# Kernel tuning notes

Measured on AMD Instinct MI355X. Metric: run time of the kernel, lower is better.

## Reference

```python
import jax, jax.numpy as jnp
import numpy as np

DIM = 2048
KV_DIM = 1024
NUM_HEADS = 16
HEAD_DIM = DIM // NUM_HEADS  # 128
EPS = 1e-6
B, LQ, LKV = 2, 4096, 1024


def _rope_cos_sin(L, d, base=10000.0):
    inv_freq = 1.0 / (base ** (np.arange(0, d, 2, dtype=np.float32) / d))  # [d/2]
    freqs = np.arange(L, dtype=np.float32)[:, None] * inv_freq[None, :]   # [L, d/2]
    emb = np.concatenate([freqs, freqs], axis=-1)                          # [L, d]
    return jnp.asarray(np.cos(emb)), jnp.asarray(np.sin(emb))


def setup_inputs() -> dict:
    key = jax.random.key(0)
    ks = jax.random.split(key, 10)
    x = jax.random.normal(ks[0], (B, LQ, DIM), dtype=jnp.float32)
    y = jax.random.normal(ks[1], (B, LKV, KV_DIM), dtype=jnp.float32)
    xc, xs = _rope_cos_sin(LQ, HEAD_DIM)
    yc, ys = _rope_cos_sin(LKV, HEAD_DIM)
    x_cos = jnp.broadcast_to(xc[None], (B, LQ, HEAD_DIM))
    x_sin = jnp.broadcast_to(xs[None], (B, LQ, HEAD_DIM))
    y_cos = jnp.broadcast_to(yc[None], (B, LKV, HEAD_DIM))
    y_sin = jnp.broadcast_to(ys[None], (B, LKV, HEAD_DIM))
    s = 0.02
    Wq = jax.random.normal(ks[2], (DIM, DIM), dtype=jnp.float32) * s
    Wk = jax.random.normal(ks[3], (DIM, KV_DIM), dtype=jnp.float32) * s
    Wv = jax.random.normal(ks[4], (DIM, KV_DIM), dtype=jnp.float32) * s
    Wo = jax.random.normal(ks[5], (DIM, DIM), dtype=jnp.float32) * s
    bq = jnp.zeros((DIM,), jnp.float32)
    bk = jnp.zeros((DIM,), jnp.float32)
    bv = jnp.zeros((DIM,), jnp.float32)
    bo = jnp.zeros((DIM,), jnp.float32)
    rmsq_w = jnp.ones((DIM,), jnp.float32)
    rmsk_w = jnp.ones((DIM,), jnp.float32)
    ln_w = jnp.ones((KV_DIM,), jnp.float32)
    ln_b = jnp.zeros((KV_DIM,), jnp.float32)
    return dict(x=x, y=y, x_cos=x_cos, x_sin=x_sin, y_cos=y_cos, y_sin=y_sin,
                Wq=Wq, bq=bq, Wk=Wk, bk=bk, Wv=Wv, bv=bv, Wo=Wo, bo=bo,
                rmsq_w=rmsq_w, rmsk_w=rmsk_w, ln_w=ln_w, ln_b=ln_b)


def _rms_norm(t, w, eps=EPS):
    return t * jax.lax.rsqrt(jnp.mean(t * t, axis=-1, keepdims=True) + eps) * w


def _layer_norm(t, w, b, eps=EPS):
    mu = jnp.mean(t, axis=-1, keepdims=True)
    var = jnp.mean(jnp.square(t - mu), axis=-1, keepdims=True)
    return (t - mu) * jax.lax.rsqrt(var + eps) * w + b


def _rotate_half(t):
    d2 = t.shape[-1] // 2
    return jnp.concatenate([-t[..., d2:], t[..., :d2]], axis=-1)


def _apply_rope(t, cos, sin):
    # t: [B, L, H, D]; cos/sin: [B, L, D] -> unsqueeze head dim (unsqueeze_dim=2)
    cos = cos[:, :, None, :]
    sin = sin[:, :, None, :]
    return t * cos + _rotate_half(t) * sin


def _block_forward(x, y, x_cos, x_sin, y_cos, y_sin,
                   Wq, bq, Wk, bk, Wv, bv, Wo, bo,
                   rmsq_w, rmsk_w, ln_w, ln_b):
    Bb, Lq, D = x.shape
    Lk = y.shape[1]
    H, Dh = NUM_HEADS, HEAD_DIM
    # y pre-norm (block-level LayerNorm)
    yn = _layer_norm(y, ln_w, ln_b)
    # projections + RMSNorm on q/k
    q = _rms_norm(x @ Wq.T + bq, rmsq_w)   # [B, Lq, D]
    k = _rms_norm(yn @ Wk.T + bk, rmsk_w)  # [B, Lk, D]
    v = yn @ Wv.T + bv                     # [B, Lk, D]
    # split heads and apply RoPE
    q = _apply_rope(q.reshape(Bb, Lq, H, Dh), x_cos, x_sin)
    k = _apply_rope(k.reshape(Bb, Lk, H, Dh), y_cos, y_sin)
    v = v.reshape(Bb, Lk, H, Dh)
    # non-causal cross attention, scale = 1/sqrt(head_dim)
    scale = 1.0 / jnp.sqrt(jnp.asarray(Dh, q.dtype))
    scores = jnp.einsum('blhd,bmhd->bhlm', q, k) * scale
    probs = jax.nn.softmax(scores, axis=-1)
    out = jnp.einsum('bhlm,bmhd->blhd', probs, v).reshape(Bb, Lq, D)
    return out @ Wo.T + bo


def reference(x, y, x_cos, x_sin, y_cos, y_sin,
              Wq, bq, Wk, bk, Wv, bv, Wo, bo,
              rmsq_w, rmsk_w, ln_w, ln_b):
    return _block_forward(x, y, x_cos, x_sin, y_cos, y_sin,
                          Wq, bq, Wk, bk, Wv, bv, Wo, bo,
                          rmsq_w, rmsk_w, ln_w, ln_b)
```

## Files before the change

### kernel.cpp

```cpp
#include <hip/hip_runtime.h>


typedef __attribute__((ext_vector_type(8))) short    short8;
typedef __attribute__((ext_vector_type(8))) unsigned short ushort8;
typedef __attribute__((ext_vector_type(4))) unsigned short ushort4v;
typedef __attribute__((ext_vector_type(4))) float    f32x4;
typedef __attribute__((ext_vector_type(16))) float   f32x16;
typedef __attribute__((ext_vector_type(4))) unsigned int uint4v;

#define DEV __device__ __forceinline__

DEV unsigned short f2bf(float f) {
  unsigned int u = __builtin_bit_cast(unsigned int, f);
  u += 0x7FFFu + ((u >> 16) & 1u);
  return (unsigned short)(u >> 16);
}
DEV float bf2f(unsigned short h) {
  return __builtin_bit_cast(float, ((unsigned int)h) << 16);
}
DEV unsigned int cvtpk_bf16(float lo, float hi) {
  unsigned int r;
  asm("v_cvt_pk_bf16_f32 %0, %1, %2" : "=v"(r) : "v"(lo), "v"(hi));
  return r;
}
DEV short8 mk8(unsigned a, unsigned b, unsigned c, unsigned d) {
  uint4v t; t.x = a; t.y = b; t.z = c; t.w = d;
  return __builtin_bit_cast(short8, t);
}

DEV void gload_lds16(const void* g, void* l) {
  __builtin_amdgcn_global_load_lds(
      (const __attribute__((address_space(1))) void*)g,
      (__attribute__((address_space(3))) void*)l, 16, 0, 0);
}

__global__ __launch_bounds__(256) void cvt_kernel(const float* __restrict__ in,
                                                  unsigned short* __restrict__ out,
                                                  int n4) {
  int idx = blockIdx.x * 256 + threadIdx.x;
  int stride = gridDim.x * 256;
  for (int i = idx; i < n4; i += stride) {
    float4 v = *(const float4*)(in + (size_t)i * 4);
    ushort4v o;
    o.x = f2bf(v.x); o.y = f2bf(v.y); o.z = f2bf(v.z); o.w = f2bf(v.w);
    *(ushort4v*)(out + (size_t)i * 4) = o;
  }
}

__global__ __launch_bounds__(256) void cvt4_kernel(const float* __restrict__ s0,
                                                   const float* __restrict__ s1,
                                                   const float* __restrict__ s2,
                                                   const float* __restrict__ s3,
                                                   unsigned short* __restrict__ d0,
                                                   unsigned short* __restrict__ d1,
                                                   unsigned short* __restrict__ d2,
                                                   unsigned short* __restrict__ d3,
                                                   int n0, int n1, int n2, int n3) {
  const int total = n0 + n1 + n2 + n3;
  int idx = blockIdx.x * 256 + threadIdx.x;
  const int stride = gridDim.x * 256;
  for (int i = idx; i < total; i += stride) {
    int j = i;
    const float* s; unsigned short* d;
    if (j < n0) { s = s0; d = d0; }
    else if ((j -= n0) < n1) { s = s1; d = d1; }
    else if ((j -= n1) < n2) { s = s2; d = d2; }
    else { j -= n2; s = s3; d = d3; }
    float4 v = *(const float4*)(s + (size_t)j * 4);
    ushort4v o;
    o.x = f2bf(v.x); o.y = f2bf(v.y); o.z = f2bf(v.z); o.w = f2bf(v.w);
    *(ushort4v*)(d + (size_t)j * 4) = o;
  }
}

__global__ __launch_bounds__(256) void ln_kernel(const float* __restrict__ y,
                                                 const float* __restrict__ w,
                                                 const float* __restrict__ b,
                                                 unsigned short* __restrict__ yn) {
  const int row = blockIdx.x;
  const int t = threadIdx.x;
  const float* yr = y + (size_t)row * 1024;
  float4 v = *(const float4*)(yr + t * 4);
  float s1 = v.x + v.y + v.z + v.w;
  float s2 = v.x * v.x + v.y * v.y + v.z * v.z + v.w * v.w;
#pragma unroll
  for (int m = 1; m < 64; m <<= 1) {
    s1 += __shfl_xor(s1, m);
    s2 += __shfl_xor(s2, m);
  }
  __shared__ float red[8];
  const int wave = t >> 6, lane = t & 63;
  if (lane == 0) { red[wave] = s1; red[4 + wave] = s2; }
  __syncthreads();
  s1 = red[0] + red[1] + red[2] + red[3];
  s2 = red[4] + red[5] + red[6] + red[7];
  const float mu = s1 * (1.0f / 1024.0f);
  const float var = s2 * (1.0f / 1024.0f) - mu * mu;
  const float rs = rsqrtf(var + 1e-6f);
  ushort4v o;
  o.x = f2bf((v.x - mu) * rs * w[t * 4 + 0] + b[t * 4 + 0]);
  o.y = f2bf((v.y - mu) * rs * w[t * 4 + 1] + b[t * 4 + 1]);
  o.z = f2bf((v.z - mu) * rs * w[t * 4 + 2] + b[t * 4 + 2]);
  o.w = f2bf((v.w - mu) * rs * w[t * 4 + 3] + b[t * 4 + 3]);
  *(ushort4v*)(yn + (size_t)row * 1024 + t * 4) = o;
}

__global__ __launch_bounds__(256) void gemm_bt(const unsigned short* __restrict__ A,
                                               const unsigned short* __restrict__ W,
                                               const float* __restrict__ bias0,
                                               const float* __restrict__ bias1,
                                               int nsplit,
                                               unsigned short* __restrict__ Cout,
                                               int M, int N, int K) {
  __shared__ __align__(16) char sA[128 * 128];
  __shared__ __align__(16) char sB[128 * 128];
  const int tid = threadIdx.x;
  const int wave = tid >> 6, lane = tid & 63;
  const int lg = lane >> 4, l15 = lane & 15;
  const int wr = wave >> 1, wc = wave & 1;
  const int m0 = blockIdx.y * 128;
  const int n0 = blockIdx.x * 128;
  const char* Ab = (const char*)A;
  const char* Wb = (const char*)W;
  const size_t ldab = (size_t)K * 2;

  f32x4 acc[4][4] = {};

  for (int kt = 0; kt < K; kt += 64) {
#pragma unroll
    for (int i = 0; i < 4; ++i) {
      const int p = (i * 256 + tid) * 16;
      const int row = p >> 7;
      const int si = (p & 127) ^ ((row & 7) << 4);
      gload_lds16(Ab + (size_t)(m0 + row) * ldab + (size_t)kt * 2 + si, sA + p);
    }
#pragma unroll
    for (int i = 0; i < 4; ++i) {
      const int p = (i * 256 + tid) * 16;
      const int row = p >> 7;
      const int si = (p & 127) ^ ((row & 7) << 4);
      gload_lds16(Wb + (size_t)(n0 + row) * ldab + (size_t)kt * 2 + si, sB + p);
    }
    __syncthreads();
#pragma unroll
    for (int ks = 0; ks < 2; ++ks) {
      const int kb = (ks * 32 + lg * 8) * 2;
      short8 af[4], bw[4];
#pragma unroll
      for (int mf = 0; mf < 4; ++mf) {
        const int row = wr * 64 + mf * 16 + l15;
        af[mf] = *(const short8*)(sA + row * 128 + (kb ^ ((row & 7) << 4)));
      }
#pragma unroll
      for (int nf = 0; nf < 4; ++nf) {
        const int row = wc * 64 + nf * 16 + l15;
        bw[nf] = *(const short8*)(sB + row * 128 + (kb ^ ((row & 7) << 4)));
      }
#pragma unroll
      for (int mf = 0; mf < 4; ++mf)
#pragma unroll
        for (int nf = 0; nf < 4; ++nf)
          acc[mf][nf] = __builtin_amdgcn_mfma_f32_16x16x32_bf16(af[mf], bw[nf],
                                                                acc[mf][nf], 0, 0, 0);
    }
    __syncthreads();
  }

#pragma unroll
  for (int nf = 0; nf < 4; ++nf) {
    const int n = n0 + wc * 64 + nf * 16 + l15;
    const float bv = (n < nsplit) ? bias0[n] : bias1[n - nsplit];
#pragma unroll
    for (int mf = 0; mf < 4; ++mf) {
      const int mB = m0 + wr * 64 + mf * 16 + lg * 4;
#pragma unroll
      for (int r = 0; r < 4; ++r)
        Cout[(size_t)(mB + r) * N + n] = f2bf(acc[mf][nf][r] + bv);
    }
  }
}

template <int EPI>
__global__ __launch_bounds__(512, 2) void gemm256(const unsigned short* __restrict__ A,
                                                  const unsigned short* __restrict__ W,
                                                  const float* __restrict__ bias,
                                                  void* __restrict__ Cout,
                                                  int M, int N, int K) {
  __shared__ __align__(16) char lds[2][4][16384];
  const int tid = threadIdx.x;
  const int wave = tid >> 6, lane = tid & 63;
  const int lg = lane >> 4, l15 = lane & 15;
  const int wm = wave >> 2, wn = wave & 3;

  const int nwg = gridDim.x;
  const int wgid = (blockIdx.x & 7) * (nwg >> 3) + (blockIdx.x >> 3);
  const int nbn = N >> 8;
  const int m0 = (wgid / nbn) * 256;
  const int n0 = (wgid % nbn) * 256;

  const char* Ab = (const char*)A;
  const char* Wb = (const char*)W;
  const size_t ld = (size_t)K * 2;
  const int NT = K >> 6;
  const int NI = NT >> 1;

  const int prow = tid >> 3;
  const int psw  = ((tid * 16) & 127) ^ ((prow & 7) << 4);
  const int pdst = tid * 16;
  const char* pAg = Ab + (size_t)(m0 + prow) * ld + psw;
  const char* pBg = Wb + (size_t)(n0 + prow) * ld + psw;

  f32x4 acc[8][4] = {};
  short8 af[4][2];
  short8 bf[4][2];

#define STG(BUF, HALF, ISB, TAU) do {                                         \
    const char* _g = ((ISB) ? pBg : pAg) + (size_t)(HALF) * 128 * ld +        \
                     (size_t)(TAU) * 128;                                     \
    char* _l = lds[BUF][(ISB) * 2 + (HALF)];                                  \
    gload_lds16(_g, _l + pdst);                                               \
    gload_lds16(_g + 64 * ld, _l + pdst + 8192);                              \
  } while (0)

#define LDA(BUF, H) do {                                                      \
    const char* _b = lds[BUF][wm];                                            \
    _Pragma("unroll") for (int mfl = 0; mfl < 4; ++mfl) {                     \
      const int _r = (H) * 64 + mfl * 16 + l15;                               \
      _Pragma("unroll") for (int ks = 0; ks < 2; ++ks)                        \
        af[mfl][ks] = *(const short8*)(_b + _r * 128 +                        \
                        ((ks * 64 + lg * 16) ^ ((_r & 7) << 4)));             \
    }                                                                         \
  } while (0)

#define LDB(BUF, G) do {                                                      \
    const char* _b = lds[BUF][2 + (wn >> 1)];                                 \
    _Pragma("unroll") for (int nfl = 0; nfl < 2; ++nfl) {                     \
      const int _r = (wn & 1) * 64 + (G) * 32 + nfl * 16 + l15;               \
      _Pragma("unroll") for (int ks = 0; ks < 2; ++ks)                        \
        bf[(G) * 2 + nfl][ks] = *(const short8*)(_b + _r * 128 +              \
                        ((ks * 64 + lg * 16) ^ ((_r & 7) << 4)));             \
    }                                                                         \
  } while (0)

#define MFMA_Q(H, G) do {                                                     \
    __builtin_amdgcn_s_setprio(1);                                            \
    _Pragma("unroll") for (int ks = 0; ks < 2; ++ks)                          \
    _Pragma("unroll") for (int mfl = 0; mfl < 4; ++mfl)                       \
    _Pragma("unroll") for (int nfl = 0; nfl < 2; ++nfl)                       \
      acc[(H) * 4 + mfl][(G) * 2 + nfl] =                                     \
        __builtin_amdgcn_mfma_f32_16x16x32_bf16(af[mfl][ks],                  \
            bf[(G) * 2 + nfl][ks], acc[(H) * 4 + mfl][(G) * 2 + nfl], 0,0,0); \
    __builtin_amdgcn_s_setprio(0);                                            \
  } while (0)

#define BAR() __builtin_amdgcn_s_barrier()
#define LGKM0() do { asm volatile("s_waitcnt lgkmcnt(0)" ::: "memory");       \
    __builtin_amdgcn_sched_barrier(0); } while (0)
#define VM4() asm volatile("s_waitcnt vmcnt(4)" ::: "memory")
#define VM0() asm volatile("s_waitcnt vmcnt(0)" ::: "memory")

  STG(0, 0, 0, 0); STG(0, 1, 0, 0); STG(0, 0, 1, 0); STG(0, 1, 1, 0);
  STG(1, 0, 1, 1); STG(1, 1, 1, 1);
  VM4(); BAR();

  for (int t = 0; t < NI - 1; ++t) {
    const int t2 = 2 * t;
    LDA(0, 0); LDB(0, 0); STG(1, 0, 0, t2 + 1);
    BAR(); LGKM0(); MFMA_Q(0, 0); BAR();
    LDB(0, 1); STG(1, 1, 0, t2 + 1);
    BAR(); LGKM0(); MFMA_Q(0, 1); BAR();
    LDA(0, 1); STG(0, 0, 1, t2 + 2);
    BAR(); LGKM0(); MFMA_Q(1, 1); BAR();
    STG(0, 1, 1, t2 + 2);
    BAR(); MFMA_Q(1, 0); VM4(); BAR();
    LDA(1, 0); LDB(1, 0); STG(0, 0, 0, t2 + 2);
    BAR(); LGKM0(); MFMA_Q(0, 0); BAR();
    LDB(1, 1); STG(0, 1, 0, t2 + 2);
    BAR(); LGKM0(); MFMA_Q(0, 1); BAR();
    LDA(1, 1); STG(1, 0, 1, t2 + 3);
    BAR(); LGKM0(); MFMA_Q(1, 1); BAR();
    STG(1, 1, 1, t2 + 3);
    BAR(); MFMA_Q(1, 0); VM4(); BAR();
  }

  LDA(0, 0); LDB(0, 0); STG(1, 0, 0, NT - 1);
  BAR(); LGKM0(); MFMA_Q(0, 0); BAR();
  LDB(0, 1); STG(1, 1, 0, NT - 1);
  BAR(); LGKM0(); MFMA_Q(0, 1); BAR();
  LDA(0, 1);
  BAR(); LGKM0(); MFMA_Q(1, 1); BAR();
  BAR(); MFMA_Q(1, 0); VM0(); BAR();
  LDA(1, 0); LDB(1, 0); LGKM0(); MFMA_Q(0, 0);
  LDB(1, 1); LGKM0(); MFMA_Q(0, 1);
  LDA(1, 1); LGKM0(); MFMA_Q(1, 1);
  MFMA_Q(1, 0);

#undef STG
#undef LDA
#undef LDB
#undef MFMA_Q
#undef BAR
#undef LGKM0
#undef VM4
#undef VM0

#pragma unroll
  for (int nf = 0; nf < 4; ++nf) {
    const int n = n0 + wn * 64 + nf * 16 + l15;
    const float bv = bias[n];
#pragma unroll
    for (int mf = 0; mf < 8; ++mf) {
      const int mB = m0 + wm * 128 + mf * 16 + lg * 4;
#pragma unroll
      for (int r = 0; r < 4; ++r) {
        const float v = acc[mf][nf][r] + bv;
        if constexpr (EPI == 0)
          ((unsigned short*)Cout)[(size_t)(mB + r) * N + n] = f2bf(v);
        else
          ((float*)Cout)[(size_t)(mB + r) * N + n] = v;
      }
    }
  }
}

__global__ __launch_bounds__(256) void rmsrope_kernel(const unsigned short* __restrict__ in,
                                                      const float* __restrict__ w,
                                                      const float* __restrict__ cs,
                                                      const float* __restrict__ sn,
                                                      unsigned short* __restrict__ out,
                                                      int L, int ldin, float scale) {
  const int row = blockIdx.x;
  const int t = threadIdx.x;
  __shared__ __align__(16) unsigned short srow[2048];
  __shared__ float red[4];
  const unsigned short* ir = in + (size_t)row * ldin;
  ushort8 v = *(const ushort8*)(ir + t * 8);
  float vals[8];
  float ss = 0.f;
#pragma unroll
  for (int j = 0; j < 8; ++j) { vals[j] = bf2f(v[j]); ss += vals[j] * vals[j]; }
  *(ushort8*)(srow + t * 8) = v;
#pragma unroll
  for (int m = 1; m < 64; m <<= 1) ss += __shfl_xor(ss, m);
  const int wave = t >> 6, lane = t & 63;
  if (lane == 0) red[wave] = ss;
  __syncthreads();
  const float tot = red[0] + red[1] + red[2] + red[3];
  const float rms = rsqrtf(tot * (1.0f / 2048.0f) + 1e-6f);

  const int n0 = t * 8;
  const int d0 = n0 & 127;
  const int hh = n0 >> 7;
  const float sign = (d0 < 64) ? -1.0f : 1.0f;
  const float* cb = cs + (size_t)row * 128 + d0;
  const float* sb = sn + (size_t)row * 128 + d0;
  ushort8 po = *(const ushort8*)(srow + (n0 ^ 64));
  ushort8 ou;
#pragma unroll
  for (int j = 0; j < 8; ++j) {
    const float self = vals[j] * rms * w[n0 + j];
    const float part = bf2f(po[j]) * rms * w[(n0 ^ 64) + j];
    ou[j] = f2bf((self * cb[j] + sign * part * sb[j]) * scale);
  }
  const int b = row / L, l = row - (row / L) * L;
  *(ushort8*)(out + (((size_t)(b * 16 + hh)) * L + l) * 128 + d0) = ou;
}

__global__ __launch_bounds__(256) void vtrans_kernel(const unsigned short* __restrict__ vpre,
                                                     unsigned short* __restrict__ vt,
                                                     int ldv) {
  const int bid = blockIdx.x;
  const int kt = bid & 15, bh = bid >> 4;
  const int h = bh & 15, b = bh >> 4;
  __shared__ unsigned short lt[64][130];
  const int t = threadIdx.x;
  const int i0 = t >> 4, c0 = (t & 15) * 8;
  const unsigned short* src = vpre + ((size_t)(b * 1024 + kt * 64)) * ldv + h * 128;
#pragma unroll
  for (int ii = 0; ii < 4; ++ii) {
    const int i = i0 + ii * 16;
    ushort8 v = *(const ushort8*)(src + (size_t)i * ldv + c0);
#pragma unroll
    for (int j = 0; j < 8; ++j) lt[i][c0 + j] = v[j];
  }
  __syncthreads();
  const int d0 = t >> 3, j0 = (t & 7) * 8;
  unsigned short* dst = vt + (size_t)bh * 128 * 1024 + kt * 64;
#pragma unroll
  for (int dd = 0; dd < 4; ++dd) {
    const int d = d0 + dd * 32;
    ushort8 o;
#pragma unroll
    for (int jj = 0; jj < 8; ++jj) o[jj] = lt[j0 + jj][d];
    *(ushort8*)(dst + (size_t)d * 1024 + j0) = o;
  }
}

__global__ __launch_bounds__(512, 2) void attn_kernel(const unsigned short* __restrict__ q,
                                                      const unsigned short* __restrict__ k,
                                                      const unsigned short* __restrict__ vt,
                                                      unsigned short* __restrict__ ao) {
  __shared__ __align__(16) char sK[2][2][64 * 256];
  __shared__ __align__(16) char sV[2][2][64 * 256];

  const int bid0 = blockIdx.x;
  const int bid = (bid0 & 7) * 64 + (bid0 >> 3);
  const int qt = bid & 15, bh = bid >> 4;
  const int tid = threadIdx.x;
  const int wave = tid >> 6, lane = tid & 63;
  const int l31 = lane & 31, hi = lane >> 5;
  const bool hib = (hi != 0);

  const unsigned short* qbase = q + (((size_t)bh * 4096) + qt * 256 + wave * 32) * 128;
  const char* kbase = (const char*)(k + (size_t)bh * 1024 * 128);
  const char* vbase = (const char*)(vt + (size_t)bh * 128 * 1024);

  short8 qb[8];
#pragma unroll
  for (int step = 0; step < 8; ++step)
    qb[step] = *(const short8*)(qbase + (size_t)l31 * 128 + step * 16 + hi * 8);

  f32x16 o[4] = {};
  f32x16 ol = {};
  const short8 vones = mk8(0x3F803F80u, 0x3F803F80u, 0x3F803F80u, 0x3F803F80u);

#define STAGE_KV(BUF, KV0) do {                                              \
    _Pragma("unroll")                                                        \
    for (int sub = 0; sub < 2; ++sub) {                                      \
      _Pragma("unroll")                                                      \
      for (int i = 0; i < 2; ++i) {                                          \
        const int p = (i * 512 + tid) * 16;                                  \
        const int row = p >> 8;                                              \
        const int si = (p & 255) ^ ((row & 15) << 4);                        \
        gload_lds16(kbase + (size_t)((KV0) + sub * 64 + row) * 256 + si,     \
                    sK[BUF][sub] + p);                                       \
      }                                                                      \
      _Pragma("unroll")                                                      \
      for (int i = 0; i < 2; ++i) {                                          \
        const int p = (i * 512 + tid) * 16;                                  \
        const int row = p >> 8;                                              \
        const int si = (p & 255) ^ ((row & 15) << 4);                        \
        const int d = 2 * row + (si >> 7);                                   \
        gload_lds16(vbase + (size_t)d * 2048 + ((KV0) + sub * 64) * 2 +      \
                    (si & 127), sV[BUF][sub] + p);                           \
      }                                                                      \
    }                                                                        \
  } while (0)

#define SOFTMAX_PV(V, SS, F) do {                                            \
    float p_[16];                                                            \
    _Pragma("unroll") for (int r = 0; r < 16; ++r) p_[r] = exp2f((SS)[r]);   \
    const unsigned w0 = cvtpk_bf16(p_[0], p_[1]),  w1 = cvtpk_bf16(p_[2], p_[3]), \
                   w2 = cvtpk_bf16(p_[4], p_[5]),  w3 = cvtpk_bf16(p_[6], p_[7]), \
                   w4 = cvtpk_bf16(p_[8], p_[9]),  w5 = cvtpk_bf16(p_[10], p_[11]),\
                   w6 = cvtpk_bf16(p_[12], p_[13]),w7 = cvtpk_bf16(p_[14], p_[15]);\
    const unsigned x0 = (unsigned)__shfl_xor((int)(hib ? w0 : w2), 32);      \
    const unsigned x1 = (unsigned)__shfl_xor((int)(hib ? w1 : w3), 32);      \
    const unsigned x2 = (unsigned)__shfl_xor((int)(hib ? w4 : w6), 32);      \
    const unsigned x3 = (unsigned)__shfl_xor((int)(hib ? w5 : w7), 32);      \
    const short8 fr0 = mk8(hib ? x0 : w0, hib ? x1 : w1,                     \
                           hib ? w2 : x0, hib ? w3 : x1);                    \
    const short8 fr1 = mk8(hib ? x2 : w4, hib ? x3 : w5,                     \
                           hib ? w6 : x2, hib ? w7 : x3);                    \
    __builtin_amdgcn_s_setprio(1);                                           \
    _Pragma("unroll") for (int kstep = 0; kstep < 2; ++kstep) {              \
      const short8 pa = kstep ? fr1 : fr0;                                   \
      const int colb = (F) * 64 + kstep * 32 + hi * 16;                      \
      _Pragma("unroll") for (int dt = 0; dt < 4; ++dt) {                     \
        const int vrow = dt * 16 + (l31 >> 1);                               \
        const int inner = (l31 & 1) * 128 + colb;                            \
        short8 vf = *(const short8*)((V) + vrow * 256 +                      \
                                     (inner ^ ((vrow & 15) << 4)));          \
        o[dt] = __builtin_amdgcn_mfma_f32_32x32x16_bf16(pa, vf, o[dt], 0,0,0);\
      }                                                                      \
      ol = __builtin_amdgcn_mfma_f32_32x32x16_bf16(pa, vones, ol, 0, 0, 0);  \
    }                                                                        \
    __builtin_amdgcn_s_setprio(0);                                           \
  } while (0)

#define SUBTILE(K, V) do {                                                   \
    f32x16 s0 = {}, s1 = {};                                                 \
    const int ksw = (l31 & 15) << 4;                                         \
    __builtin_amdgcn_s_setprio(1);                                           \
    _Pragma("unroll") for (int step = 0; step < 8; ++step) {                 \
      const int cb2 = step * 32 + hi * 16;                                   \
      short8 kf0 = *(const short8*)((K) + l31 * 256 + (cb2 ^ ksw));          \
      short8 kf1 = *(const short8*)((K) + (32 + l31) * 256 + (cb2 ^ ksw));   \
      s0 = __builtin_amdgcn_mfma_f32_32x32x16_bf16(kf0, qb[step], s0, 0,0,0);\
      s1 = __builtin_amdgcn_mfma_f32_32x32x16_bf16(kf1, qb[step], s1, 0,0,0);\
    }                                                                        \
    __builtin_amdgcn_s_setprio(0);                                           \
    SOFTMAX_PV(V, s0, 0);                                                    \
    SOFTMAX_PV(V, s1, 1);                                                    \
  } while (0)

#define TILE(BUF) do {                                                       \
    SUBTILE(sK[BUF][0], sV[BUF][0]);                                         \
    SUBTILE(sK[BUF][1], sV[BUF][1]);                                         \
  } while (0)

  STAGE_KV(0, 0);
  __syncthreads();

#pragma unroll 1
  for (int kt2 = 0; kt2 < 4; ++kt2) {
    STAGE_KV(1, (2 * kt2 + 1) * 128);
    TILE(0);
    __syncthreads();
    if (kt2 < 3) STAGE_KV(0, (2 * kt2 + 2) * 128);
    TILE(1);
    __syncthreads();
  }
#undef STAGE_KV
#undef SOFTMAX_PV
#undef SUBTILE
#undef TILE

  const int b = bh >> 4, h = bh & 15;
#pragma unroll
  for (int r = 0; r < 16; ++r) {
    const int crow = (r & 3) + 8 * (r >> 2) + 4 * hi;
    const float inv = 1.0f / ol[r];
    const int qg = qt * 256 + wave * 32 + crow;
    const size_t orow = ((size_t)b * 4096 + qg) * 2048 + h * 128;
#pragma unroll
    for (int dt = 0; dt < 4; ++dt)
      ao[orow + dt * 32 + l31] = f2bf(o[dt][r] * inv);
  }
}

extern "C" void kernel_launch(void* const* d_in, const int* in_sizes, int n_in,
                              void* d_out, int out_size, void* d_ws, size_t ws_size,
                              hipStream_t stream) {
  (void)in_sizes; (void)n_in; (void)out_size; (void)ws_size;
  const float* x      = (const float*)d_in[0];
  const float* y      = (const float*)d_in[1];
  const float* x_cos  = (const float*)d_in[2];
  const float* x_sin  = (const float*)d_in[3];
  const float* y_cos  = (const float*)d_in[4];
  const float* y_sin  = (const float*)d_in[5];
  const float* Wq     = (const float*)d_in[6];
  const float* bq     = (const float*)d_in[7];
  const float* Wk     = (const float*)d_in[8];
  const float* bk     = (const float*)d_in[9];
  const float* Wv     = (const float*)d_in[10];
  const float* bv     = (const float*)d_in[11];
  const float* Wo     = (const float*)d_in[12];
  const float* bo     = (const float*)d_in[13];
  const float* rmsq_w = (const float*)d_in[14];
  const float* rmsk_w = (const float*)d_in[15];
  const float* ln_w   = (const float*)d_in[16];
  const float* ln_b   = (const float*)d_in[17];

  char* ws = (char*)d_ws;
  unsigned short* xb    = (unsigned short*)(ws + 0);
  unsigned short* Wqb   = (unsigned short*)(ws + 33554432);
  unsigned short* Wkb   = (unsigned short*)(ws + 41943040);
  unsigned short* Wvb   = (unsigned short*)(ws + 46137344);
  unsigned short* Wob   = (unsigned short*)(ws + 50331648);
  unsigned short* ynb   = (unsigned short*)(ws + 58720256);
  unsigned short* kvpre = (unsigned short*)(ws + 62914560);
  unsigned short* qpre  = (unsigned short*)(ws + 62914560);
  unsigned short* qr    = (unsigned short*)(ws + 96468992);
  unsigned short* kr    = (unsigned short*)(ws + 130023424);
  unsigned short* vt    = (unsigned short*)(ws + 138412032);
  unsigned short* ao    = xb;

  const float qscale = 1.4426950408889634f * 0.08838834764831843f;

  cvt_kernel<<<2048, 256, 0, stream>>>(x, xb, (2 * 4096 * 2048) / 4);
  cvt4_kernel<<<2048, 256, 0, stream>>>(Wq, Wk, Wv, Wo, Wqb, Wkb, Wvb, Wob,
                                        (2048 * 2048) / 4, (2048 * 1024) / 4,
                                        (2048 * 1024) / 4, (2048 * 2048) / 4);
  ln_kernel<<<2048, 256, 0, stream>>>(y, ln_w, ln_b, ynb);

  dim3 gKV(32, 16);
  gemm_bt<<<gKV, 256, 0, stream>>>(ynb, Wkb, bk, bv, 2048, kvpre, 2048, 4096, 1024);
  rmsrope_kernel<<<2048, 256, 0, stream>>>(kvpre, rmsk_w, y_cos, y_sin, kr, 1024, 4096, 1.0f);
  vtrans_kernel<<<512, 256, 0, stream>>>(kvpre + 2048, vt, 4096);

  gemm256<0><<<256, 512, 0, stream>>>(xb, Wqb, bq, qpre, 8192, 2048, 2048);
  rmsrope_kernel<<<8192, 256, 0, stream>>>(qpre, rmsq_w, x_cos, x_sin, qr, 4096, 2048, qscale);

  attn_kernel<<<512, 512, 0, stream>>>(qr, kr, vt, ao);

  gemm256<1><<<256, 512, 0, stream>>>(ao, Wob, bo, (float*)d_out, 8192, 2048, 2048);
}
```

Measured before the change: 306.7 us.

## Compute softmax row sums with VALU adds and batch QK MFMAs per tile

```diff
diff --git a/kernel.cpp b/kernel.cpp
--- a/kernel.cpp
+++ b/kernel.cpp
@@ -421,8 +421,7 @@
     qb[step] = *(const short8*)(qbase + (size_t)l31 * 128 + step * 16 + hi * 8);
 
   f32x16 o[4] = {};
-  f32x16 ol = {};
-  const short8 vones = mk8(0x3F803F80u, 0x3F803F80u, 0x3F803F80u, 0x3F803F80u);
+  float lsum = 0.f;
 
 #define STAGE_KV(BUF, KV0) do {                                              \
     _Pragma("unroll")                                                        \
@@ -447,9 +446,22 @@
     }                                                                        \
   } while (0)
 
+#define QK(K, S0, S1) do {                                                   \
+    const int ksw = (l31 & 15) << 4;                                         \
+    _Pragma("unroll") for (int step = 0; step < 8; ++step) {                 \
+      const int cb2 = step * 32 + hi * 16;                                   \
+      short8 kf0 = *(const short8*)((K) + l31 * 256 + (cb2 ^ ksw));          \
+      short8 kf1 = *(const short8*)((K) + (32 + l31) * 256 + (cb2 ^ ksw));   \
+      S0 = __builtin_amdgcn_mfma_f32_32x32x16_bf16(kf0, qb[step], S0, 0,0,0);\
+      S1 = __builtin_amdgcn_mfma_f32_32x32x16_bf16(kf1, qb[step], S1, 0,0,0);\
+    }                                                                        \
+  } while (0)
+
 #define SOFTMAX_PV(V, SS, F) do {                                            \
     float p_[16];                                                            \
     _Pragma("unroll") for (int r = 0; r < 16; ++r) p_[r] = exp2f((SS)[r]);   \
+    lsum += (((p_[0]+p_[1])+(p_[2]+p_[3])) + ((p_[4]+p_[5])+(p_[6]+p_[7])))  \
+          + (((p_[8]+p_[9])+(p_[10]+p_[11])) + ((p_[12]+p_[13])+(p_[14]+p_[15])));\
     const unsigned w0 = cvtpk_bf16(p_[0], p_[1]),  w1 = cvtpk_bf16(p_[2], p_[3]), \
                    w2 = cvtpk_bf16(p_[4], p_[5]),  w3 = cvtpk_bf16(p_[6], p_[7]), \
                    w4 = cvtpk_bf16(p_[8], p_[9]),  w5 = cvtpk_bf16(p_[10], p_[11]),\
@@ -462,7 +474,6 @@
                            hib ? w2 : x0, hib ? w3 : x1);                    \
     const short8 fr1 = mk8(hib ? x2 : w4, hib ? x3 : w5,                     \
                            hib ? w6 : x2, hib ? w7 : x3);                    \
-    __builtin_amdgcn_s_setprio(1);                                           \
     _Pragma("unroll") for (int kstep = 0; kstep < 2; ++kstep) {              \
       const short8 pa = kstep ? fr1 : fr0;                                   \
       const int colb = (F) * 64 + kstep * 32 + hi * 16;                      \
@@ -473,30 +484,17 @@
                                      (inner ^ ((vrow & 15) << 4)));          \
         o[dt] = __builtin_amdgcn_mfma_f32_32x32x16_bf16(pa, vf, o[dt], 0,0,0);\
       }                                                                      \
-      ol = __builtin_amdgcn_mfma_f32_32x32x16_bf16(pa, vones, ol, 0, 0, 0);  \
     }                                                                        \
-    __builtin_amdgcn_s_setprio(0);                                           \
-  } while (0)
-
-#define SUBTILE(K, V) do {                                                   \
-    f32x16 s0 = {}, s1 = {};                                                 \
-    const int ksw = (l31 & 15) << 4;                                         \
-    __builtin_amdgcn_s_setprio(1);                                           \
-    _Pragma("unroll") for (int step = 0; step < 8; ++step) {                 \
-      const int cb2 = step * 32 + hi * 16;                                   \
-      short8 kf0 = *(const short8*)((K) + l31 * 256 + (cb2 ^ ksw));          \
-      short8 kf1 = *(const short8*)((K) + (32 + l31) * 256 + (cb2 ^ ksw));   \
-      s0 = __builtin_amdgcn_mfma_f32_32x32x16_bf16(kf0, qb[step], s0, 0,0,0);\
-      s1 = __builtin_amdgcn_mfma_f32_32x32x16_bf16(kf1, qb[step], s1, 0,0,0);\
-    }                                                                        \
-    __builtin_amdgcn_s_setprio(0);                                           \
-    SOFTMAX_PV(V, s0, 0);                                                    \
-    SOFTMAX_PV(V, s1, 1);                                                    \
   } while (0)
 
 #define TILE(BUF) do {                                                       \
-    SUBTILE(sK[BUF][0], sV[BUF][0]);                                         \
-    SUBTILE(sK[BUF][1], sV[BUF][1]);                                         \
+    f32x16 s0 = {}, s1 = {}, s2 = {}, s3 = {};                               \
+    QK(sK[BUF][0], s0, s1);                                                  \
+    QK(sK[BUF][1], s2, s3);                                                  \
+    SOFTMAX_PV(sV[BUF][0], s0, 0);                                           \
+    SOFTMAX_PV(sV[BUF][0], s1, 1);                                           \
+    SOFTMAX_PV(sV[BUF][1], s2, 0);                                           \
+    SOFTMAX_PV(sV[BUF][1], s3, 1);                                           \
   } while (0)
 
   STAGE_KV(0, 0);
@@ -512,15 +510,17 @@
     __syncthreads();
   }
 #undef STAGE_KV
+#undef QK
 #undef SOFTMAX_PV
-#undef SUBTILE
 #undef TILE
 
+  lsum += __shfl_xor(lsum, 32);
+  const float linv = 1.0f / lsum;
   const int b = bh >> 4, h = bh & 15;
 #pragma unroll
   for (int r = 0; r < 16; ++r) {
     const int crow = (r & 3) + 8 * (r >> 2) + 4 * hi;
-    const float inv = 1.0f / ol[r];
+    const float inv = __shfl(linv, crow);
     const int qg = qt * 256 + wave * 32 + crow;
     const size_t orow = ((size_t)b * 4096 + qg) * 2048 + h * 128;
 #pragma unroll
```

Result: no change. 306.7 us (-0.0%).
